# Kernel optimization log

Measured on AMD Instinct MI355X. Metric: run time of the kernel, lower is better.

The kernel has to match this reference:

```python
import jax, jax.numpy as jnp
import numpy as np

B, T, I, H, L = 256, 256, 256, 1024, 128


def setup_inputs() -> dict:
    key = jax.random.key(0)
    ks = jax.random.split(key, 10)
    s = 0.05
    return {
        "z": jax.random.normal(ks[0], (B, L), dtype=jnp.float32),
        "seq_len": T,
        "target": jax.random.uniform(ks[1], (B, T, I), dtype=jnp.float32),
        "W_z2h": jax.random.normal(ks[2], (H, L), dtype=jnp.float32) * s,
        "b_z2h": jnp.zeros((H,), dtype=jnp.float32),
        "W_ih": jax.random.normal(ks[3], (3 * H, I), dtype=jnp.float32) * s,
        "W_hh": jax.random.normal(ks[4], (3 * H, H), dtype=jnp.float32) * s,
        "b_ih": jnp.zeros((3 * H,), dtype=jnp.float32),
        "b_hh": jnp.zeros((3 * H,), dtype=jnp.float32),
        "W_out": jax.random.normal(ks[5], (I, H), dtype=jnp.float32) * s,
        "b_out": jnp.zeros((I,), dtype=jnp.float32),
    }


def reference(z, seq_len, target, W_z2h, b_z2h, W_ih, W_hh, b_ih, b_hh, W_out, b_out):
    # h0 = tanh(Linear(z))  -- [B, H]
    h0 = jnp.tanh(z @ W_z2h.T + b_z2h)
    # Precompute input-side gate pre-activations for all steps: [T, B, 3H]
    xg = jnp.einsum("bti,gi->tbg", target, W_ih) + b_ih

    hdim = h0.shape[-1]

    def step(h, xg_t):
        hg = h @ W_hh.T + b_hh  # [B, 3H]
        xr, xz, xn = jnp.split(xg_t, 3, axis=-1)
        hr, hz, hn = jnp.split(hg, 3, axis=-1)
        r = jax.nn.sigmoid(xr + hr)
        zg = jax.nn.sigmoid(xz + hz)
        n = jnp.tanh(xn + r * hn)
        h_new = (1.0 - zg) * n + zg * h
        y = jax.nn.sigmoid(h_new @ W_out.T + b_out)  # [B, I]
        return h_new, y

    _, ys = jax.lax.scan(step, h0, xg)  # ys: [T, B, I]
    return jnp.transpose(ys, (1, 0, 2))  # [B, T, I]
```

## Files before the change

### kernel.cpp

```cpp
#include <hip/hip_runtime.h>

#define BB 256
#define TT 256
#define II 256
#define HH 1024
#define LL 128
#define K1 1280
#define GN 3072

#define RP 49
#define GP 17
#define PP 20

typedef short s8v    __attribute__((ext_vector_type(8)));
typedef float f32x4  __attribute__((ext_vector_type(4)));
typedef float f4v    __attribute__((ext_vector_type(4)));
typedef unsigned long long u64;

__device__ __forceinline__ unsigned short f2bf(float f) {
    unsigned u = __float_as_uint(f);
    u += 0x7fffu + ((u >> 16) & 1u);
    return (unsigned short)(u >> 16);
}
__device__ __forceinline__ float bf2f(unsigned short h) {
    return __uint_as_float(((unsigned)h) << 16);
}
__device__ __forceinline__ float sigm(float x) { return 1.0f / (1.0f + __expf(-x)); }

__device__ __forceinline__ s8v cvt8(const float* __restrict__ p) {
    const f4v lo = *(const f4v*)p;
    const f4v hi = *(const f4v*)(p + 4);
    s8v r;
    r[0] = (short)f2bf(lo[0]); r[1] = (short)f2bf(lo[1]);
    r[2] = (short)f2bf(lo[2]); r[3] = (short)f2bf(lo[3]);
    r[4] = (short)f2bf(hi[0]); r[5] = (short)f2bf(hi[1]);
    r[6] = (short)f2bf(hi[2]); r[7] = (short)f2bf(hi[3]);
    return r;
}

__device__ __forceinline__ s8v hload16a(const unsigned short* p) {
    union { u64 q[2]; s8v v; } u;
    u.q[0] = __hip_atomic_load((const u64*)p, __ATOMIC_RELAXED, __HIP_MEMORY_SCOPE_AGENT);
    u.q[1] = __hip_atomic_load((const u64*)p + 1, __ATOMIC_RELAXED, __HIP_MEMORY_SCOPE_AGENT);
    return u.v;
}
template<int FRESH> __device__ __forceinline__ s8v ld16h(const unsigned short* p) {
    if constexpr (FRESH) return *(const s8v*)p;
    else return hload16a(p);
}
template<int FRESH> __device__ __forceinline__ u64 ld8h(const unsigned short* p) {
    if constexpr (FRESH) return *(const u64*)p;
    else return __hip_atomic_load((const u64*)p, __ATOMIC_RELAXED, __HIP_MEMORY_SCOPE_AGENT);
}
__device__ __forceinline__ void st8h(unsigned short* p, u64 v) {
    __hip_atomic_store((u64*)p, v, __ATOMIC_RELAXED, __HIP_MEMORY_SCOPE_AGENT);
}

__device__ __forceinline__ void poll_pair(const unsigned* p, unsigned t) {
    if (t == 0) return;
    int guard = 0;
    for (;;) {
        u64 v = __hip_atomic_load((const u64*)p, __ATOMIC_RELAXED, __HIP_MEMORY_SCOPE_AGENT);
        if ((unsigned)v >= t && (unsigned)(v >> 32) >= t) return;
        __builtin_amdgcn_s_sleep(1);
        if (++guard > (1 << 17)) return;
    }
}
__device__ __forceinline__ void poll_range16(const unsigned* p0, int lr, unsigned t) {
    if (t == 0) return;
    int guard = 0;
    for (;;) {
        unsigned v = __hip_atomic_load(p0 + lr, __ATOMIC_RELAXED, __HIP_MEMORY_SCOPE_AGENT);
        if (__ballot(v >= t) == ~0ull) break;
        __builtin_amdgcn_s_sleep(1);
        if (++guard > (1 << 17)) break;
    }
    asm volatile("" ::: "memory");
}
__device__ __forceinline__ void poll_range64(const unsigned* p0, int lane, unsigned t) {
    if (t == 0) return;
    int guard = 0;
    for (;;) {
        unsigned v = __hip_atomic_load(p0 + lane, __ATOMIC_RELAXED, __HIP_MEMORY_SCOPE_AGENT);
        if (__ballot(v >= t) == ~0ull) break;
        __builtin_amdgcn_s_sleep(1);
        if (++guard > (1 << 17)) break;
    }
    asm volatile("" ::: "memory");
}

__global__ void k_prep_w(const float* __restrict__ Whh, const float* __restrict__ Wih,
                         unsigned short* __restrict__ Wperm) {
    int o = blockIdx.x;
    int ntt = o / 48, q = o - ntt * 48;
    int gate = q >> 4, j = ntt * 16 + (q & 15);
    int src = gate * HH + j;
    const float* sh = Whh + (size_t)src * HH;
    const float* si = Wih + (size_t)src * II;
    unsigned short* dst = Wperm + (size_t)o * K1;
    for (int k = threadIdx.x; k < K1; k += 256)
        dst[k] = f2bf(k < HH ? sh[k] : si[k - HH]);
}

__global__ void k_prep_misc(const float* __restrict__ bih, const float* __restrict__ bhh,
                            const float* __restrict__ Wout,
                            float* __restrict__ bihp, float* __restrict__ bhhp,
                            unsigned short* __restrict__ Woutb) {
    int idx = blockIdx.x * 256 + threadIdx.x;
    if (idx < GN) {
        int ntt = idx / 48, q = idx - ntt * 48;
        int gate = q >> 4, j = ntt * 16 + (q & 15);
        int src = gate * HH + j;
        bihp[idx] = bih[src];
        bhhp[idx] = bhh[src];
    }
    for (size_t i = (size_t)blockIdx.x * 256 + threadIdx.x; i < (size_t)II * HH;
         i += (size_t)gridDim.x * 256)
        Woutb[i] = f2bf(Wout[i]);
}

__global__ void k_h0(const float* __restrict__ z, const float* __restrict__ Wz,
                     const float* __restrict__ bz, unsigned short* __restrict__ hbuf) {
    int b = blockIdx.x;
    int j0 = threadIdx.x * 4;
    const f4v* zr = (const f4v*)(z + (size_t)b * LL);
    u64 packed = 0;
#pragma unroll
    for (int jj = 0; jj < 4; ++jj) {
        int j = j0 + jj;
        const f4v* wr = (const f4v*)(Wz + (size_t)j * LL);
        float s = bz[j];
#pragma unroll
        for (int i = 0; i < LL / 4; ++i) {
            f4v a = zr[i], w = wr[i];
            s += a[0] * w[0] + a[1] * w[1] + a[2] * w[2] + a[3] * w[3];
        }
        packed |= (u64)f2bf(tanhf(s)) << (16 * jj);
    }
    *(u64*)(hbuf + (size_t)b * HH + j0) = packed;
}

template<int FRESH>
__device__ __forceinline__ void proj_tile(
    const unsigned short* hb, const unsigned short* __restrict__ Woutb,
    float* __restrict__ out, float (*pred)[16 * PP],
    int brow, int io, int wave, int lane, int lr, int lk, int tp, float boutv) {
    f32x4 oa = {0.f, 0.f, 0.f, 0.f};
    const unsigned short* ap = hb + (size_t)(brow + lr) * HH + (wave << 8) + lk;
    const unsigned short* wp = Woutb + (size_t)(io * 16 + lr) * HH + (wave << 8) + lk;
#pragma unroll
    for (int ks = 0; ks < 8; ++ks) {
        s8v a = ld16h<FRESH>(ap + ks * 32);
        s8v w = *(const s8v*)(wp + ks * 32);
        oa = __builtin_amdgcn_mfma_f32_16x16x32_bf16(a, w, oa, 0, 0, 0);
    }
    if (wave >= 1) {
#pragma unroll
        for (int r = 0; r < 4; ++r)
            pred[wave - 1][(((lane >> 4) << 2) + r) * PP + lr] = oa[r];
    }
    __syncthreads();
    if (wave == 0) {
#pragma unroll
        for (int r = 0; r < 4; ++r) {
            int rw = ((lane >> 4) << 2) + r;
            int idx = rw * PP + lr;
            float v = oa[r] + pred[0][idx] + pred[1][idx] + pred[2][idx] + boutv;
            out[(size_t)(brow + rw) * (TT * II) + (size_t)tp * II + io * 16 + lr] = sigm(v);
        }
    }
    __syncthreads();
}

template<int FRESH>
__device__ void run(const float* __restrict__ tgt, const unsigned short* __restrict__ Wperm,
                    const float* __restrict__ bihp, const float* __restrict__ bhhp,
                    unsigned short* hbuf, const unsigned short* __restrict__ Woutb,
                    const float* __restrict__ bout, float* __restrict__ out,
                    unsigned* flags,
                    float (*red)[64 * RP], float* gxn, float (*pred)[16 * PP]) {
    const int tid = threadIdx.x;
    const int wave = tid >> 6, lane = tid & 63;
    const int lr = lane & 15;
    const int lk = (lane >> 4) << 3;
    const int bid = blockIdx.x;
    const int m = bid >> 6, nt = bid & 63;
    const int brow = m * 64 + (nt >> 4) * 16;
    const int io = nt & 15;
    const float boutv = bout[io * 16 + lr];

    const int eb = lane;
    const int j4 = wave << 2;
    const int ob = nt * 48;
    float bir[4], biz[4], bixn[4], bihn[4];
#pragma unroll
    for (int jj = 0; jj < 4; ++jj) {
        int j = j4 + jj;
        bir[jj]  = bihp[ob + j] + bhhp[ob + j];
        biz[jj]  = bihp[ob + 16 + j] + bhhp[ob + 16 + j];
        bixn[jj] = bihp[ob + 32 + j];
        bihn[jj] = bhhp[ob + 32 + j];
    }

    s8v wreg[30];
    if (wave == 3) {
#pragma unroll
        for (int ks = 0; ks < 2; ++ks)
#pragma unroll
            for (int ni = 0; ni < 3; ++ni)
                wreg[ks * 3 + ni] = *(const s8v*)(Wperm +
                    (size_t)(nt * 48 + ni * 16 + lr) * K1 + 960 + ks * 32 + lk);
#pragma unroll
        for (int ks = 0; ks < 8; ++ks)
#pragma unroll
            for (int ni = 0; ni < 3; ++ni)
                wreg[6 + ks * 3 + ni] = *(const s8v*)(Wperm +
                    (size_t)(nt * 48 + ni * 16 + lr) * K1 + HH + ks * 32 + lk);
    } else {
#pragma unroll
        for (int ks = 0; ks < 10; ++ks)
#pragma unroll
            for (int ni = 0; ni < 3; ++ni)
                wreg[ks * 3 + ni] = *(const s8v*)(Wperm +
                    (size_t)(nt * 48 + ni * 16 + lr) * K1 + wave * 320 + ks * 32 + lk);
    }

    unsigned* gflags = flags + (m << 6);

    for (int t = 0; t < TT; ++t) {
        const unsigned short* hcur = hbuf + (size_t)(FRESH ? t : (t % 3)) * (BB * HH);
        unsigned short* hnxt = hbuf + (size_t)(FRESH ? (t + 1) : ((t + 1) % 3)) * (BB * HH);

        f32x4 acc[12];
#pragma unroll
        for (int i = 0; i < 12; ++i) acc[i] = (f32x4){0.f, 0.f, 0.f, 0.f};
        f32x4 accx[4];
#pragma unroll
        for (int i = 0; i < 4; ++i) accx[i] = (f32x4){0.f, 0.f, 0.f, 0.f};

        if (wave == 3) {
#pragma unroll
            for (int ks = 0; ks < 8; ++ks) {
                s8v xa[4];
#pragma unroll
                for (int mi = 0; mi < 4; ++mi)
                    xa[mi] = cvt8(tgt +
                        ((size_t)(m * 64 + mi * 16 + lr) * TT + t) * II + ks * 32 + lk);
#pragma unroll
                for (int mi = 0; mi < 4; ++mi) {
                    acc[mi * 3 + 0] = __builtin_amdgcn_mfma_f32_16x16x32_bf16(
                        xa[mi], wreg[6 + ks * 3 + 0], acc[mi * 3 + 0], 0, 0, 0);
                    acc[mi * 3 + 1] = __builtin_amdgcn_mfma_f32_16x16x32_bf16(
                        xa[mi], wreg[6 + ks * 3 + 1], acc[mi * 3 + 1], 0, 0, 0);
                    accx[mi] = __builtin_amdgcn_mfma_f32_16x16x32_bf16(
                        xa[mi], wreg[6 + ks * 3 + 2], accx[mi], 0, 0, 0);
                }
            }
        }

        if constexpr (!FRESH) {
            if (wave == 0) poll_range64(gflags, lane, (unsigned)t);
            __syncthreads();
        }

        if (wave < 3) {
            const unsigned* fp = gflags + wave * 20;
            poll_pair(fp, (unsigned)t);
#pragma unroll
            for (int ci = 0; ci < 10; ++ci) {
                s8v a[4];
#pragma unroll
                for (int mi = 0; mi < 4; ++mi)
                    a[mi] = ld16h<FRESH>(hcur +
                        (size_t)(m * 64 + mi * 16 + lr) * HH + wave * 320 + ci * 32 + lk);
                if (ci < 9) poll_pair(fp + 2 * (ci + 1), (unsigned)t);
#pragma unroll
                for (int mi = 0; mi < 4; ++mi)
#pragma unroll
                    for (int ni = 0; ni < 3; ++ni)
                        acc[mi * 3 + ni] = __builtin_amdgcn_mfma_f32_16x16x32_bf16(
                            a[mi], wreg[ci * 3 + ni], acc[mi * 3 + ni], 0, 0, 0);
            }
        } else {
            poll_pair(gflags + 60, (unsigned)t);
#pragma unroll
            for (int ks = 0; ks < 2; ++ks) {
                s8v a[4];
#pragma unroll
                for (int mi = 0; mi < 4; ++mi)
                    a[mi] = ld16h<FRESH>(hcur +
                        (size_t)(m * 64 + mi * 16 + lr) * HH + 960 + ks * 32 + lk);
                if (ks == 0) poll_pair(gflags + 62, (unsigned)t);
#pragma unroll
                for (int mi = 0; mi < 4; ++mi)
#pragma unroll
                    for (int ni = 0; ni < 3; ++ni)
                        acc[mi * 3 + ni] = __builtin_amdgcn_mfma_f32_16x16x32_bf16(
                            a[mi], wreg[ks * 3 + ni], acc[mi * 3 + ni], 0, 0, 0);
            }
#pragma unroll
            for (int mi = 0; mi < 4; ++mi)
#pragma unroll
                for (int r = 0; r < 4; ++r)
                    gxn[(mi * 16 + ((lane >> 4) << 2) + r) * GP + lr] = accx[mi][r];
        }

        {
            float* s = &red[wave][0];
#pragma unroll
            for (int mi = 0; mi < 4; ++mi)
#pragma unroll
                for (int ni = 0; ni < 3; ++ni)
#pragma unroll
                    for (int r = 0; r < 4; ++r)
                        s[(mi * 16 + ((lane >> 4) << 2) + r) * RP + ni * 16 + lr] =
                            acc[mi * 3 + ni][r];
        }
        __syncthreads();

        {
            const int bg = m * 64 + eb;
            const int jg = nt * 16 + j4;
            u64 hold8 = ld8h<FRESH>(hcur + (size_t)bg * HH + jg);
            u64 packed = 0;
#pragma unroll
            for (int jj = 0; jj < 4; ++jj) {
                int c = j4 + jj;
                int i0 = eb * RP + c;
                float ghr = red[0][i0] + red[1][i0] + red[2][i0] + red[3][i0];
                float ghz = red[0][i0 + 16] + red[1][i0 + 16] + red[2][i0 + 16] + red[3][i0 + 16];
                float ghn = red[0][i0 + 32] + red[1][i0 + 32] + red[2][i0 + 32] + red[3][i0 + 32];
                float gx  = gxn[eb * GP + c];
                float r   = sigm(ghr + bir[jj]);
                float zg  = sigm(ghz + biz[jj]);
                float n   = tanhf(gx + bixn[jj] + r * (ghn + bihn[jj]));
                float ho  = bf2f((unsigned short)(hold8 >> (16 * jj)));
                packed |= (u64)f2bf((1.f - zg) * n + zg * ho) << (16 * jj);
            }
            st8h(hnxt + (size_t)bg * HH + jg, packed);
        }

        asm volatile("s_waitcnt vmcnt(0)" ::: "memory");
        __syncthreads();
        if (tid == 0)
            __hip_atomic_store(gflags + nt, (unsigned)(t + 1), __ATOMIC_RELAXED,
                               __HIP_MEMORY_SCOPE_AGENT);

        if (t > 0) {
            poll_range16(gflags + (wave << 4), lr, (unsigned)t);
            proj_tile<FRESH>(hcur, Woutb, out, pred, brow, io, wave, lane, lr, lk,
                             t - 1, boutv);
        }
    }

    poll_range16(gflags + (wave << 4), lr, (unsigned)TT);
    proj_tile<FRESH>(hbuf + (size_t)(FRESH ? TT : (TT % 3)) * (BB * HH),
                     Woutb, out, pred, brow, io, wave, lane, lr, lk, TT - 1, boutv);
}

__global__ __launch_bounds__(256, 1) void dec_main(
    const float* __restrict__ tgt, const unsigned short* __restrict__ Wperm,
    const float* __restrict__ bihp, const float* __restrict__ bhhp,
    unsigned short* hbuf, const unsigned short* __restrict__ Woutb,
    const float* __restrict__ bout, float* __restrict__ out,
    unsigned* flags, int fresh) {
    __shared__ float red[4][64 * RP];
    __shared__ float gxn[64 * GP];
    __shared__ float pred[3][16 * PP];
    if (fresh)
        run<1>(tgt, Wperm, bihp, bhhp, hbuf, Woutb, bout, out, flags, red, gxn, pred);
    else
        run<0>(tgt, Wperm, bihp, bhhp, hbuf, Woutb, bout, out, flags, red, gxn, pred);
}

extern "C" void kernel_launch(void* const* d_in, const int* in_sizes, int n_in,
                              void* d_out, int out_size, void* d_ws, size_t ws_size,
                              hipStream_t stream) {
    const float* z    = (const float*)d_in[0];
    const float* tgt  = (const float*)d_in[2];
    const float* Wz2h = (const float*)d_in[3];
    const float* bz2h = (const float*)d_in[4];
    const float* Wih  = (const float*)d_in[5];
    const float* Whh  = (const float*)d_in[6];
    const float* bih  = (const float*)d_in[7];
    const float* bhh  = (const float*)d_in[8];
    const float* Wout = (const float*)d_in[9];
    const float* bout = (const float*)d_in[10];
    float* out = (float*)d_out;

    char* ws = (char*)d_ws;
    unsigned short* Wperm = (unsigned short*)ws;
    float* bihp           = (float*)(ws + 7864320);
    float* bhhp           = (float*)(ws + 7876608);
    unsigned short* Woutb = (unsigned short*)(ws + 7888896);
    unsigned* flags       = (unsigned*)(ws + 8413184);
    unsigned short* hbuf  = (unsigned short*)(ws + 8415232);

    const size_t need_big = 8415232ull + 257ull * 524288ull;
    const int fresh = (ws_size >= need_big) ? 1 : 0;

    hipMemsetAsync((void*)flags, 0, 1024, stream);
    hipLaunchKernelGGL(k_prep_w, dim3(GN), dim3(256), 0, stream, Whh, Wih, Wperm);
    hipLaunchKernelGGL(k_prep_misc, dim3(1024), dim3(256), 0, stream, bih, bhh, Wout,
                       bihp, bhhp, Woutb);
    hipLaunchKernelGGL(k_h0, dim3(BB), dim3(256), 0, stream, z, Wz2h, bz2h, hbuf);
    hipLaunchKernelGGL(dec_main, dim3(256), dim3(256), 0, stream,
                       tgt, Wperm, bihp, bhhp, hbuf, Woutb, bout, out, flags, fresh);
}
```

Measured before the change: 5.542 ms.

## Partition GRU batch into XCD-local groups with per-group flag sync

Splits the persistent GRU kernel into 8 batch groups of 32 rows, indexed by blockIdx&7 so that each group's 32 blocks are expected to land on one XCD. At startup every block records its hardware XCC ID and the group checks it is colocated. If so, hidden-state stores become plain (non-atomic) writes, relying on the shared L2. Each block now computes 32 hidden units for 32 batch rows and streams W_hh/W_ih from memory every step instead of keeping them in registers. Fine-grained per-chunk polling is replaced by one group-wide wait, so cross-XCD coherence traffic shrinks, at the cost of more weight loads per step and a grid-wide startup barrier.

```diff
diff --git a/kernel.cpp b/kernel.cpp
--- a/kernel.cpp
+++ b/kernel.cpp
@@ -7,22 +7,24 @@
 #define LL 128
 #define K1 1280
 #define GN 3072
-
-#define RP 49
-#define GP 17
+#define BBHH (BB * HH)
+
+#define RP2 97
+#define GP2 33
 #define PP 20
 
 typedef short s8v    __attribute__((ext_vector_type(8)));
 typedef float f32x4  __attribute__((ext_vector_type(4)));
 typedef float f4v    __attribute__((ext_vector_type(4)));
 typedef unsigned long long u64;
-
-__device__ __forceinline__ unsigned short f2bf(float f) {
+typedef unsigned short us;
+
+__device__ __forceinline__ us f2bf(float f) {
     unsigned u = __float_as_uint(f);
     u += 0x7fffu + ((u >> 16) & 1u);
-    return (unsigned short)(u >> 16);
-}
-__device__ __forceinline__ float bf2f(unsigned short h) {
+    return (us)(u >> 16);
+}
+__device__ __forceinline__ float bf2f(us h) {
     return __uint_as_float(((unsigned)h) << 16);
 }
 __device__ __forceinline__ float sigm(float x) { return 1.0f / (1.0f + __expf(-x)); }
@@ -38,66 +40,52 @@
     return r;
 }
 
-__device__ __forceinline__ s8v hload16a(const unsigned short* p) {
+__device__ __forceinline__ s8v hload16a(const us* p) {
     union { u64 q[2]; s8v v; } u;
     u.q[0] = __hip_atomic_load((const u64*)p, __ATOMIC_RELAXED, __HIP_MEMORY_SCOPE_AGENT);
     u.q[1] = __hip_atomic_load((const u64*)p + 1, __ATOMIC_RELAXED, __HIP_MEMORY_SCOPE_AGENT);
     return u.v;
 }
-template<int FRESH> __device__ __forceinline__ s8v ld16h(const unsigned short* p) {
+template<int FRESH> __device__ __forceinline__ s8v ld16h(const us* p) {
     if constexpr (FRESH) return *(const s8v*)p;
     else return hload16a(p);
 }
-template<int FRESH> __device__ __forceinline__ u64 ld8h(const unsigned short* p) {
+template<int FRESH> __device__ __forceinline__ u64 ld8h(const us* p) {
     if constexpr (FRESH) return *(const u64*)p;
     else return __hip_atomic_load((const u64*)p, __ATOMIC_RELAXED, __HIP_MEMORY_SCOPE_AGENT);
 }
-__device__ __forceinline__ void st8h(unsigned short* p, u64 v) {
-    __hip_atomic_store((u64*)p, v, __ATOMIC_RELAXED, __HIP_MEMORY_SCOPE_AGENT);
-}
-
-__device__ __forceinline__ void poll_pair(const unsigned* p, unsigned t) {
+template<int LOCAL> __device__ __forceinline__ void h_store8(us* p, u64 v) {
+    if constexpr (LOCAL) *(u64*)p = v;
+    else __hip_atomic_store((u64*)p, v, __ATOMIC_RELAXED, __HIP_MEMORY_SCOPE_AGENT);
+}
+__device__ __forceinline__ void flag_store(unsigned* p, unsigned v) {
+    __hip_atomic_store(p, v, __ATOMIC_RELAXED, __HIP_MEMORY_SCOPE_AGENT);
+}
+__device__ __forceinline__ unsigned flag_probe(unsigned* p) {
+    return __hip_atomic_load(p, __ATOMIC_RELAXED, __HIP_MEMORY_SCOPE_AGENT);
+}
+__device__ __forceinline__ void group_wait(unsigned* gf, int lane, unsigned t) {
     if (t == 0) return;
     int guard = 0;
     for (;;) {
-        u64 v = __hip_atomic_load((const u64*)p, __ATOMIC_RELAXED, __HIP_MEMORY_SCOPE_AGENT);
-        if ((unsigned)v >= t && (unsigned)(v >> 32) >= t) return;
-        __builtin_amdgcn_s_sleep(1);
-        if (++guard > (1 << 17)) return;
-    }
-}
-__device__ __forceinline__ void poll_range16(const unsigned* p0, int lr, unsigned t) {
-    if (t == 0) return;
-    int guard = 0;
-    for (;;) {
-        unsigned v = __hip_atomic_load(p0 + lr, __ATOMIC_RELAXED, __HIP_MEMORY_SCOPE_AGENT);
+        unsigned v = t;
+        if (lane < 32) v = flag_probe(gf + lane);
         if (__ballot(v >= t) == ~0ull) break;
         __builtin_amdgcn_s_sleep(1);
-        if (++guard > (1 << 17)) break;
+        if (++guard > (1 << 18)) break;
     }
     asm volatile("" ::: "memory");
 }
-__device__ __forceinline__ void poll_range64(const unsigned* p0, int lane, unsigned t) {
-    if (t == 0) return;
-    int guard = 0;
-    for (;;) {
-        unsigned v = __hip_atomic_load(p0 + lane, __ATOMIC_RELAXED, __HIP_MEMORY_SCOPE_AGENT);
-        if (__ballot(v >= t) == ~0ull) break;
-        __builtin_amdgcn_s_sleep(1);
-        if (++guard > (1 << 17)) break;
-    }
-    asm volatile("" ::: "memory");
-}
 
 __global__ void k_prep_w(const float* __restrict__ Whh, const float* __restrict__ Wih,
-                         unsigned short* __restrict__ Wperm) {
+                         us* __restrict__ Wperm) {
     int o = blockIdx.x;
-    int ntt = o / 48, q = o - ntt * 48;
-    int gate = q >> 4, j = ntt * 16 + (q & 15);
-    int src = gate * HH + j;
+    int ntt = o / 96, q = o - ntt * 96;
+    int gate = q >> 5, jj = q & 31;
+    int src = gate * HH + ntt * 32 + jj;
     const float* sh = Whh + (size_t)src * HH;
     const float* si = Wih + (size_t)src * II;
-    unsigned short* dst = Wperm + (size_t)o * K1;
+    us* dst = Wperm + (size_t)o * K1;
     for (int k = threadIdx.x; k < K1; k += 256)
         dst[k] = f2bf(k < HH ? sh[k] : si[k - HH]);
 }
@@ -105,12 +93,12 @@
 __global__ void k_prep_misc(const float* __restrict__ bih, const float* __restrict__ bhh,
                             const float* __restrict__ Wout,
                             float* __restrict__ bihp, float* __restrict__ bhhp,
-                            unsigned short* __restrict__ Woutb) {
+                            us* __restrict__ Woutb) {
     int idx = blockIdx.x * 256 + threadIdx.x;
     if (idx < GN) {
-        int ntt = idx / 48, q = idx - ntt * 48;
-        int gate = q >> 4, j = ntt * 16 + (q & 15);
-        int src = gate * HH + j;
+        int ntt = idx / 96, q = idx - ntt * 96;
+        int gate = q >> 5, jj = q & 31;
+        int src = gate * HH + ntt * 32 + jj;
         bihp[idx] = bih[src];
         bhhp[idx] = bhh[src];
     }
@@ -120,7 +108,7 @@
 }
 
 __global__ void k_h0(const float* __restrict__ z, const float* __restrict__ Wz,
-                     const float* __restrict__ bz, unsigned short* __restrict__ hbuf) {
+                     const float* __restrict__ bz, us* __restrict__ hbuf) {
     int b = blockIdx.x;
     int j0 = threadIdx.x * 4;
     const f4v* zr = (const f4v*)(z + (size_t)b * LL);
@@ -142,12 +130,12 @@
 
 template<int FRESH>
 __device__ __forceinline__ void proj_tile(
-    const unsigned short* hb, const unsigned short* __restrict__ Woutb,
+    const us* hb, const us* __restrict__ Woutb,
     float* __restrict__ out, float (*pred)[16 * PP],
-    int brow, int io, int wave, int lane, int lr, int lk, int tp, float boutv) {
+    int brow, int it, int wave, int lane, int lr, int lk, int tp, float boutv) {
     f32x4 oa = {0.f, 0.f, 0.f, 0.f};
-    const unsigned short* ap = hb + (size_t)(brow + lr) * HH + (wave << 8) + lk;
-    const unsigned short* wp = Woutb + (size_t)(io * 16 + lr) * HH + (wave << 8) + lk;
+    const us* ap = hb + (size_t)(brow + lr) * HH + (wave << 8) + lk;
+    const us* wp = Woutb + (size_t)(it * 16 + lr) * HH + (wave << 8) + lk;
 #pragma unroll
     for (int ks = 0; ks < 8; ++ks) {
         s8v a = ld16h<FRESH>(ap + ks * 32);
@@ -166,70 +154,47 @@
             int rw = ((lane >> 4) << 2) + r;
             int idx = rw * PP + lr;
             float v = oa[r] + pred[0][idx] + pred[1][idx] + pred[2][idx] + boutv;
-            out[(size_t)(brow + rw) * (TT * II) + (size_t)tp * II + io * 16 + lr] = sigm(v);
+            out[(size_t)(brow + rw) * (TT * II) + (size_t)tp * II + it * 16 + lr] = sigm(v);
         }
     }
     __syncthreads();
 }
 
-template<int FRESH>
-__device__ void run(const float* __restrict__ tgt, const unsigned short* __restrict__ Wperm,
-                    const float* __restrict__ bihp, const float* __restrict__ bhhp,
-                    unsigned short* hbuf, const unsigned short* __restrict__ Woutb,
-                    const float* __restrict__ bout, float* __restrict__ out,
-                    unsigned* flags,
-                    float (*red)[64 * RP], float* gxn, float (*pred)[16 * PP]) {
+template<int LOCAL, int FRESH>
+__device__ void run9(const float* __restrict__ tgt, const us* __restrict__ Wperm,
+                     const float* __restrict__ bihp, const float* __restrict__ bhhp,
+                     us* hbuf, const us* __restrict__ Woutb,
+                     const float* __restrict__ bout, float* __restrict__ out,
+                     unsigned* flags,
+                     float (*red)[32 * RP2], float* gxn, float (*pred)[16 * PP]) {
     const int tid = threadIdx.x;
     const int wave = tid >> 6, lane = tid & 63;
     const int lr = lane & 15;
     const int lk = (lane >> 4) << 3;
+    const int hi4 = ((lane >> 4) << 2);
     const int bid = blockIdx.x;
-    const int m = bid >> 6, nt = bid & 63;
-    const int brow = m * 64 + (nt >> 4) * 16;
-    const int io = nt & 15;
-    const float boutv = bout[io * 16 + lr];
-
-    const int eb = lane;
-    const int j4 = wave << 2;
-    const int ob = nt * 48;
+    const int g = bid & 7, nt = bid >> 3;
+    const int bt = nt >> 4, it = nt & 15;
+    const int brow = g * 32 + bt * 16;
+    const float boutv = bout[it * 16 + lr];
+
+    const int eb = tid & 31, jq = tid >> 5;
+    const int ob = nt * 96;
     float bir[4], biz[4], bixn[4], bihn[4];
 #pragma unroll
     for (int jj = 0; jj < 4; ++jj) {
-        int j = j4 + jj;
-        bir[jj]  = bihp[ob + j] + bhhp[ob + j];
-        biz[jj]  = bihp[ob + 16 + j] + bhhp[ob + 16 + j];
-        bixn[jj] = bihp[ob + 32 + j];
-        bihn[jj] = bhhp[ob + 32 + j];
-    }
-
-    s8v wreg[30];
-    if (wave == 3) {
-#pragma unroll
-        for (int ks = 0; ks < 2; ++ks)
-#pragma unroll
-            for (int ni = 0; ni < 3; ++ni)
-                wreg[ks * 3 + ni] = *(const s8v*)(Wperm +
-                    (size_t)(nt * 48 + ni * 16 + lr) * K1 + 960 + ks * 32 + lk);
-#pragma unroll
-        for (int ks = 0; ks < 8; ++ks)
-#pragma unroll
-            for (int ni = 0; ni < 3; ++ni)
-                wreg[6 + ks * 3 + ni] = *(const s8v*)(Wperm +
-                    (size_t)(nt * 48 + ni * 16 + lr) * K1 + HH + ks * 32 + lk);
-    } else {
-#pragma unroll
-        for (int ks = 0; ks < 10; ++ks)
-#pragma unroll
-            for (int ni = 0; ni < 3; ++ni)
-                wreg[ks * 3 + ni] = *(const s8v*)(Wperm +
-                    (size_t)(nt * 48 + ni * 16 + lr) * K1 + wave * 320 + ks * 32 + lk);
-    }
-
-    unsigned* gflags = flags + (m << 6);
+        int lj = jq * 4 + jj;
+        bir[jj]  = bihp[ob + lj] + bhhp[ob + lj];
+        biz[jj]  = bihp[ob + 32 + lj] + bhhp[ob + 32 + lj];
+        bixn[jj] = bihp[ob + 64 + lj];
+        bihn[jj] = bhhp[ob + 64 + lj];
+    }
+
+    unsigned* gflags = flags + (g << 6);
 
     for (int t = 0; t < TT; ++t) {
-        const unsigned short* hcur = hbuf + (size_t)(FRESH ? t : (t % 3)) * (BB * HH);
-        unsigned short* hnxt = hbuf + (size_t)(FRESH ? (t + 1) : ((t + 1) % 3)) * (BB * HH);
+        const us* hcur = hbuf + (size_t)(FRESH ? t : (t % 3)) * BBHH;
+        us* hnxt = hbuf + (size_t)(FRESH ? (t + 1) : ((t + 1) % 3)) * BBHH;
 
         f32x4 acc[12];
 #pragma unroll
@@ -241,136 +206,172 @@
         if (wave == 3) {
 #pragma unroll
             for (int ks = 0; ks < 8; ++ks) {
-                s8v xa[4];
-#pragma unroll
-                for (int mi = 0; mi < 4; ++mi)
-                    xa[mi] = cvt8(tgt +
-                        ((size_t)(m * 64 + mi * 16 + lr) * TT + t) * II + ks * 32 + lk);
-#pragma unroll
-                for (int mi = 0; mi < 4; ++mi) {
-                    acc[mi * 3 + 0] = __builtin_amdgcn_mfma_f32_16x16x32_bf16(
-                        xa[mi], wreg[6 + ks * 3 + 0], acc[mi * 3 + 0], 0, 0, 0);
-                    acc[mi * 3 + 1] = __builtin_amdgcn_mfma_f32_16x16x32_bf16(
-                        xa[mi], wreg[6 + ks * 3 + 1], acc[mi * 3 + 1], 0, 0, 0);
-                    accx[mi] = __builtin_amdgcn_mfma_f32_16x16x32_bf16(
-                        xa[mi], wreg[6 + ks * 3 + 2], accx[mi], 0, 0, 0);
+                const int k0 = ks * 32 + lk;
+                s8v xa[2], w[6];
+#pragma unroll
+                for (int mi = 0; mi < 2; ++mi)
+                    xa[mi] = cvt8(tgt + ((size_t)(g * 32 + mi * 16 + lr) * TT + t) * II + k0);
+#pragma unroll
+                for (int ni = 0; ni < 6; ++ni)
+                    w[ni] = *(const s8v*)(Wperm + (size_t)(ob + ni * 16 + lr) * K1 + HH + k0);
+#pragma unroll
+                for (int mi = 0; mi < 2; ++mi) {
+#pragma unroll
+                    for (int ni = 0; ni < 4; ++ni)
+                        acc[mi * 6 + ni] = __builtin_amdgcn_mfma_f32_16x16x32_bf16(
+                            xa[mi], w[ni], acc[mi * 6 + ni], 0, 0, 0);
+                    accx[mi * 2 + 0] = __builtin_amdgcn_mfma_f32_16x16x32_bf16(
+                        xa[mi], w[4], accx[mi * 2 + 0], 0, 0, 0);
+                    accx[mi * 2 + 1] = __builtin_amdgcn_mfma_f32_16x16x32_bf16(
+                        xa[mi], w[5], accx[mi * 2 + 1], 0, 0, 0);
                 }
             }
         }
 
-        if constexpr (!FRESH) {
-            if (wave == 0) poll_range64(gflags, lane, (unsigned)t);
-            __syncthreads();
-        }
+        if (wave == 0) group_wait(gflags, lane, (unsigned)t);
+        __syncthreads();
 
         if (wave < 3) {
-            const unsigned* fp = gflags + wave * 20;
-            poll_pair(fp, (unsigned)t);
 #pragma unroll
             for (int ci = 0; ci < 10; ++ci) {
-                s8v a[4];
-#pragma unroll
-                for (int mi = 0; mi < 4; ++mi)
-                    a[mi] = ld16h<FRESH>(hcur +
-                        (size_t)(m * 64 + mi * 16 + lr) * HH + wave * 320 + ci * 32 + lk);
-                if (ci < 9) poll_pair(fp + 2 * (ci + 1), (unsigned)t);
-#pragma unroll
-                for (int mi = 0; mi < 4; ++mi)
-#pragma unroll
-                    for (int ni = 0; ni < 3; ++ni)
-                        acc[mi * 3 + ni] = __builtin_amdgcn_mfma_f32_16x16x32_bf16(
-                            a[mi], wreg[ci * 3 + ni], acc[mi * 3 + ni], 0, 0, 0);
+                const int k0 = wave * 320 + ci * 32 + lk;
+                s8v a[2], w[6];
+#pragma unroll
+                for (int mi = 0; mi < 2; ++mi)
+                    a[mi] = ld16h<FRESH>(hcur + (size_t)(g * 32 + mi * 16 + lr) * HH + k0);
+#pragma unroll
+                for (int ni = 0; ni < 6; ++ni)
+                    w[ni] = *(const s8v*)(Wperm + (size_t)(ob + ni * 16 + lr) * K1 + k0);
+#pragma unroll
+                for (int mi = 0; mi < 2; ++mi)
+#pragma unroll
+                    for (int ni = 0; ni < 6; ++ni)
+                        acc[mi * 6 + ni] = __builtin_amdgcn_mfma_f32_16x16x32_bf16(
+                            a[mi], w[ni], acc[mi * 6 + ni], 0, 0, 0);
             }
         } else {
-            poll_pair(gflags + 60, (unsigned)t);
 #pragma unroll
             for (int ks = 0; ks < 2; ++ks) {
-                s8v a[4];
-#pragma unroll
-                for (int mi = 0; mi < 4; ++mi)
-                    a[mi] = ld16h<FRESH>(hcur +
-                        (size_t)(m * 64 + mi * 16 + lr) * HH + 960 + ks * 32 + lk);
-                if (ks == 0) poll_pair(gflags + 62, (unsigned)t);
-#pragma unroll
-                for (int mi = 0; mi < 4; ++mi)
-#pragma unroll
-                    for (int ni = 0; ni < 3; ++ni)
-                        acc[mi * 3 + ni] = __builtin_amdgcn_mfma_f32_16x16x32_bf16(
-                            a[mi], wreg[ks * 3 + ni], acc[mi * 3 + ni], 0, 0, 0);
+                const int k0 = 960 + ks * 32 + lk;
+                s8v a[2], w[6];
+#pragma unroll
+                for (int mi = 0; mi < 2; ++mi)
+                    a[mi] = ld16h<FRESH>(hcur + (size_t)(g * 32 + mi * 16 + lr) * HH + k0);
+#pragma unroll
+                for (int ni = 0; ni < 6; ++ni)
+                    w[ni] = *(const s8v*)(Wperm + (size_t)(ob + ni * 16 + lr) * K1 + k0);
+#pragma unroll
+                for (int mi = 0; mi < 2; ++mi)
+#pragma unroll
+                    for (int ni = 0; ni < 6; ++ni)
+                        acc[mi * 6 + ni] = __builtin_amdgcn_mfma_f32_16x16x32_bf16(
+                            a[mi], w[ni], acc[mi * 6 + ni], 0, 0, 0);
             }
 #pragma unroll
-            for (int mi = 0; mi < 4; ++mi)
-#pragma unroll
-                for (int r = 0; r < 4; ++r)
-                    gxn[(mi * 16 + ((lane >> 4) << 2) + r) * GP + lr] = accx[mi][r];
+            for (int mi = 0; mi < 2; ++mi)
+#pragma unroll
+                for (int n2 = 0; n2 < 2; ++n2)
+#pragma unroll
+                    for (int r = 0; r < 4; ++r)
+                        gxn[(mi * 16 + hi4 + r) * GP2 + n2 * 16 + lr] = accx[mi * 2 + n2][r];
         }
 
         {
             float* s = &red[wave][0];
 #pragma unroll
-            for (int mi = 0; mi < 4; ++mi)
-#pragma unroll
-                for (int ni = 0; ni < 3; ++ni)
+            for (int mi = 0; mi < 2; ++mi)
+#pragma unroll
+                for (int ni = 0; ni < 6; ++ni)
 #pragma unroll
                     for (int r = 0; r < 4; ++r)
-                        s[(mi * 16 + ((lane >> 4) << 2) + r) * RP + ni * 16 + lr] =
-                            acc[mi * 3 + ni][r];
+                        s[(mi * 16 + hi4 + r) * RP2 + ni * 16 + lr] = acc[mi * 6 + ni][r];
         }
         __syncthreads();
 
         {
-            const int bg = m * 64 + eb;
-            const int jg = nt * 16 + j4;
-            u64 hold8 = ld8h<FRESH>(hcur + (size_t)bg * HH + jg);
+            const int bg = g * 32 + eb;
+            const int jbase = nt * 32 + jq * 4;
+            u64 hold8 = ld8h<FRESH>(hcur + (size_t)bg * HH + jbase);
             u64 packed = 0;
 #pragma unroll
             for (int jj = 0; jj < 4; ++jj) {
-                int c = j4 + jj;
-                int i0 = eb * RP + c;
-                float ghr = red[0][i0] + red[1][i0] + red[2][i0] + red[3][i0];
-                float ghz = red[0][i0 + 16] + red[1][i0 + 16] + red[2][i0 + 16] + red[3][i0 + 16];
-                float ghn = red[0][i0 + 32] + red[1][i0 + 32] + red[2][i0 + 32] + red[3][i0 + 32];
-                float gx  = gxn[eb * GP + c];
+                int lj = jq * 4 + jj;
+                float ghr = red[0][eb * RP2 + lj] + red[1][eb * RP2 + lj] +
+                            red[2][eb * RP2 + lj] + red[3][eb * RP2 + lj];
+                float ghz = red[0][eb * RP2 + 32 + lj] + red[1][eb * RP2 + 32 + lj] +
+                            red[2][eb * RP2 + 32 + lj] + red[3][eb * RP2 + 32 + lj];
+                float ghn = red[0][eb * RP2 + 64 + lj] + red[1][eb * RP2 + 64 + lj] +
+                            red[2][eb * RP2 + 64 + lj] + red[3][eb * RP2 + 64 + lj];
+                float gx  = gxn[eb * GP2 + lj];
                 float r   = sigm(ghr + bir[jj]);
                 float zg  = sigm(ghz + biz[jj]);
                 float n   = tanhf(gx + bixn[jj] + r * (ghn + bihn[jj]));
-                float ho  = bf2f((unsigned short)(hold8 >> (16 * jj)));
+                float ho  = bf2f((us)(hold8 >> (16 * jj)));
                 packed |= (u64)f2bf((1.f - zg) * n + zg * ho) << (16 * jj);
             }
-            st8h(hnxt + (size_t)bg * HH + jg, packed);
+            h_store8<LOCAL>(hnxt + (size_t)bg * HH + jbase, packed);
         }
 
         asm volatile("s_waitcnt vmcnt(0)" ::: "memory");
         __syncthreads();
-        if (tid == 0)
-            __hip_atomic_store(gflags + nt, (unsigned)(t + 1), __ATOMIC_RELAXED,
-                               __HIP_MEMORY_SCOPE_AGENT);
-
-        if (t > 0) {
-            poll_range16(gflags + (wave << 4), lr, (unsigned)t);
-            proj_tile<FRESH>(hcur, Woutb, out, pred, brow, io, wave, lane, lr, lk,
+        if (tid == 0) flag_store(gflags + nt, (unsigned)(t + 1));
+
+        if (t > 0)
+            proj_tile<FRESH>(hcur, Woutb, out, pred, brow, it, wave, lane, lr, lk,
                              t - 1, boutv);
-        }
-    }
-
-    poll_range16(gflags + (wave << 4), lr, (unsigned)TT);
-    proj_tile<FRESH>(hbuf + (size_t)(FRESH ? TT : (TT % 3)) * (BB * HH),
-                     Woutb, out, pred, brow, io, wave, lane, lr, lk, TT - 1, boutv);
-}
-
-__global__ __launch_bounds__(256, 1) void dec_main(
-    const float* __restrict__ tgt, const unsigned short* __restrict__ Wperm,
+    }
+
+    if (wave == 0) group_wait(gflags, lane, (unsigned)TT);
+    __syncthreads();
+    proj_tile<FRESH>(hbuf + (size_t)(FRESH ? TT : (TT % 3)) * BBHH,
+                     Woutb, out, pred, brow, it, wave, lane, lr, lk, TT - 1, boutv);
+}
+
+__global__ __launch_bounds__(256, 1) void dec10(
+    const float* __restrict__ tgt, const us* __restrict__ Wperm,
     const float* __restrict__ bihp, const float* __restrict__ bhhp,
-    unsigned short* hbuf, const unsigned short* __restrict__ Woutb,
+    us* hbuf, const us* __restrict__ Woutb,
     const float* __restrict__ bout, float* __restrict__ out,
-    unsigned* flags, int fresh) {
-    __shared__ float red[4][64 * RP];
-    __shared__ float gxn[64 * GP];
+    unsigned* xcdarr, unsigned* gstart, unsigned* flags, int fresh) {
+    __shared__ float red[4][32 * RP2];
+    __shared__ float gxn[32 * GP2];
     __shared__ float pred[3][16 * PP];
-    if (fresh)
-        run<1>(tgt, Wperm, bihp, bhhp, hbuf, Woutb, bout, out, flags, red, gxn, pred);
-    else
-        run<0>(tgt, Wperm, bihp, bhhp, hbuf, Woutb, bout, out, flags, red, gxn, pred);
+    __shared__ int lflag;
+
+    const int tid = threadIdx.x, bid = blockIdx.x;
+    const int g = bid & 7;
+
+    unsigned myxcd;
+    asm volatile("s_getreg_b32 %0, hwreg(HW_REG_XCC_ID)" : "=s"(myxcd));
+
+    if (tid == 0) {
+        __hip_atomic_store(xcdarr + bid, myxcd + 1u, __ATOMIC_RELAXED, __HIP_MEMORY_SCOPE_AGENT);
+        __hip_atomic_fetch_add(gstart, 1u, __ATOMIC_RELEASE, __HIP_MEMORY_SCOPE_AGENT);
+        int guard = 0;
+        while (__hip_atomic_load(gstart, __ATOMIC_ACQUIRE, __HIP_MEMORY_SCOPE_AGENT) < 256u) {
+            __builtin_amdgcn_s_sleep(8);
+            if (++guard > (1 << 20)) break;
+        }
+    }
+    __syncthreads();
+    if (tid < 64) {
+        unsigned v = (tid < 32)
+            ? __hip_atomic_load(xcdarr + g + 8 * tid, __ATOMIC_RELAXED, __HIP_MEMORY_SCOPE_AGENT)
+            : (myxcd + 1u);
+        unsigned long long b = __ballot(v == myxcd + 1u);
+        if (tid == 0) lflag = (b == ~0ull) ? 1 : 0;
+    }
+    __syncthreads();
+    const int local = lflag;
+
+    if (fresh) {
+        if (local)
+            run9<1, 1>(tgt, Wperm, bihp, bhhp, hbuf, Woutb, bout, out, flags, red, gxn, pred);
+        else
+            run9<0, 1>(tgt, Wperm, bihp, bhhp, hbuf, Woutb, bout, out, flags, red, gxn, pred);
+    } else {
+        run9<0, 0>(tgt, Wperm, bihp, bhhp, hbuf, Woutb, bout, out, flags, red, gxn, pred);
+    }
 }
 
 extern "C" void kernel_launch(void* const* d_in, const int* in_sizes, int n_in,
@@ -389,21 +390,25 @@
     float* out = (float*)d_out;
 
     char* ws = (char*)d_ws;
-    unsigned short* Wperm = (unsigned short*)ws;
-    float* bihp           = (float*)(ws + 7864320);
-    float* bhhp           = (float*)(ws + 7876608);
-    unsigned short* Woutb = (unsigned short*)(ws + 7888896);
-    unsigned* flags       = (unsigned*)(ws + 8413184);
-    unsigned short* hbuf  = (unsigned short*)(ws + 8415232);
-
-    const size_t need_big = 8415232ull + 257ull * 524288ull;
+    us* Wperm        = (us*)ws;
+    float* bihp      = (float*)(ws + 7864320);
+    float* bhhp      = (float*)(ws + 7876608);
+    us* Woutb        = (us*)(ws + 7888896);
+    unsigned* xcdarr = (unsigned*)(ws + 8413184);
+    unsigned* gstart = (unsigned*)(ws + 8414208);
+    unsigned* flags  = (unsigned*)(ws + 8414336);
+    us* hbuf         = (us*)(ws + 8416512);
+
+    const size_t slotB = (size_t)BBHH * 2;
+    const size_t need_big = 8416512ull + 257ull * slotB;
     const int fresh = (ws_size >= need_big) ? 1 : 0;
 
-    hipMemsetAsync((void*)flags, 0, 1024, stream);
+    hipMemsetAsync((void*)xcdarr, 0, 3328, stream);
     hipLaunchKernelGGL(k_prep_w, dim3(GN), dim3(256), 0, stream, Whh, Wih, Wperm);
     hipLaunchKernelGGL(k_prep_misc, dim3(1024), dim3(256), 0, stream, bih, bhh, Wout,
                        bihp, bhhp, Woutb);
     hipLaunchKernelGGL(k_h0, dim3(BB), dim3(256), 0, stream, z, Wz2h, bz2h, hbuf);
-    hipLaunchKernelGGL(dec_main, dim3(256), dim3(256), 0, stream,
-                       tgt, Wperm, bihp, bhhp, hbuf, Woutb, bout, out, flags, fresh);
-}
+    hipLaunchKernelGGL(dec10, dim3(256), dim3(256), 0, stream,
+                       tgt, Wperm, bihp, bhhp, hbuf, Woutb, bout, out,
+                       xcdarr, gstart, flags, fresh);
+}
```

Result: slower. 6.438 ms (+16.2%).
